# Kernel optimization log

Hardware: AMD Instinct MI355X
Metric: run time of the kernel (lower is better)

Reference implementation:

```python
import jax, jax.numpy as jnp
import numpy as np

B = 16384      # batch
H = 1024       # latent_dim
C = 2          # output_dim (classes)
PPC = 24       # prototypes per class
P = C * PPC    # 48 total prototypes
EPS = 1e-4


def setup_inputs() -> dict:
    key = jax.random.key(0)
    k1, k2, k3, k4, k5 = jax.random.split(key, 5)
    specific_user = jax.random.normal(k1, (B, H), jnp.float32)
    shared_user = jax.random.normal(k2, (B, H), jnp.float32)
    prototype_vectors = jax.random.normal(k3, (P, H), jnp.float32)
    # last_layer weight set by set_last_layer_incorrect_connection(-0.5):
    # +1 for the prototype's own class, -0.5 elsewhere; shape [C, P]
    cls = np.arange(P) // PPC
    ident = (cls[None, :] == np.arange(C)[:, None]).astype(np.float32)
    last_layer_w = jnp.asarray(ident * 1.0 + (1.0 - ident) * (-0.5))
    # nn.Bilinear(H, H, 1): weight [1, H, H], bias [1]
    bilinear_w = jax.random.normal(k4, (1, H, H), jnp.float32) / np.sqrt(H)
    bilinear_b = jax.random.normal(k5, (1,), jnp.float32) * 0.01
    return {
        "specific_user": specific_user,
        "shared_user": shared_user,
        "prototype_vectors": prototype_vectors,
        "last_layer_w": last_layer_w,
        "bilinear_w": bilinear_w,
        "bilinear_b": bilinear_b,
        "flag": 1,
    }


def reference(specific_user, shared_user, prototype_vectors, last_layer_w,
              bilinear_w, bilinear_b, flag):
    # prototype_distances: squared euclid via mm + norms, then log-similarity
    x2 = jnp.sum(specific_user ** 2, axis=1, keepdims=True)          # [B,1]
    p2 = jnp.sum(prototype_vectors ** 2, axis=1)                     # [P]
    distance = -2.0 * (specific_user @ prototype_vectors.T) + x2 + p2[None, :]  # [B,P]
    similarity = jnp.log((distance + 1.0) / (distance + EPS))        # [B,P]
    logits = similarity @ last_layer_w.T                             # [B,C]

    # select the class's 24 prototypes (flag picks class 1 or 0; static int)
    idx = 1 if flag else 0
    sub = prototype_vectors.reshape(C, PPC, H)[idx]                  # [PPC,H]

    # prototype_subgraph_distances: per original broadcast, each row of
    # all_sim is the batch-mean of the log-similarity -> constant over batch.
    s2 = jnp.sum(sub ** 2, axis=1)                                   # [PPC]
    d = -2.0 * (specific_user @ sub.T) + x2 + s2[None, :]            # [B,PPC]
    sim = jnp.mean(jnp.log((d + 1.0) / (d + EPS)), axis=0)           # [PPC]
    jstar = jnp.argmax(sim)                                          # scalar
    chosen_proto = jnp.broadcast_to(sub[jstar], specific_user.shape) # [B,H]

    # nn.Bilinear(chosen_proto, shared_user) -> [B,1]
    pos = jnp.einsum('bi,ij,bj->b', chosen_proto, bilinear_w[0], shared_user)[:, None] + bilinear_b
    return (pos, shared_user, logits, distance)
```

## Files before the change

kernel.cpp:

```cpp
#include <hip/hip_runtime.h>
#include <hip/hip_bf16.h>

#define BATCH 16384
#define HD    1024
#define NP    48
#define PPC   24
#define EPSV  1e-4f

typedef __attribute__((ext_vector_type(8))) short  short8;
typedef __attribute__((ext_vector_type(4))) float  floatx4;

__device__ __forceinline__ float b2f(unsigned short s) {
    union { unsigned u; float f; } c; c.u = ((unsigned)s) << 16; return c.f;
}
__device__ __forceinline__ unsigned short f2bu(float f) {
    __hip_bfloat16 h = __float2bfloat16(f);
    union { __hip_bfloat16 h; unsigned short u; } c; c.h = h; return c.u;
}

__global__ __launch_bounds__(64) void k_prep(const float* __restrict__ proto,
                                             unsigned short* __restrict__ phi,
                                             unsigned short* __restrict__ plo,
                                             float* __restrict__ p2) {
    const int p = blockIdx.x;
    const int lane = threadIdx.x;
    const float* row = proto + (size_t)p * HD;
    float acc = 0.f;
    for (int k = lane; k < HD; k += 64) {
        const float f = row[k];
        acc += f * f;
        const unsigned short h = f2bu(f);
        phi[(size_t)p * HD + k] = h;
        plo[(size_t)p * HD + k] = f2bu(f - b2f(h));
    }
#pragma unroll
    for (int m = 32; m >= 1; m >>= 1) acc += __shfl_xor(acc, m, 64);
    if (lane == 0) p2[p] = acc;
}

__global__ __launch_bounds__(256) void k_main(
    const float* __restrict__ x,
    const unsigned short* __restrict__ phi,
    const unsigned short* __restrict__ plo,
    const float* __restrict__ llw,
    const float* __restrict__ p2,
    float* __restrict__ partials,
    float* __restrict__ out_logits,
    float* __restrict__ out_dist)
{
    __shared__ float cs[NP];
    const int wave = threadIdx.x >> 6;
    const int lane = threadIdx.x & 63;
    const int quad = lane >> 4;
    const int lr   = lane & 15;
    const int rb   = (blockIdx.x * 4 + wave) * 16;

    if (threadIdx.x < NP) cs[threadIdx.x] = 0.f;
    __syncthreads();

    const float* xr = x + (size_t)(rb + lr) * HD + quad * 8;
    const unsigned short* ph0 = phi + (size_t)lr * HD + quad * 8;
    const unsigned short* ph1 = ph0 + 16 * HD;
    const unsigned short* ph2 = ph0 + 32 * HD;
    const unsigned short* pl0 = plo + (size_t)lr * HD + quad * 8;
    const unsigned short* pl1 = pl0 + 16 * HD;
    const unsigned short* pl2 = pl0 + 32 * HD;

    floatx4 acc0 = {0.f, 0.f, 0.f, 0.f};
    floatx4 acc1 = {0.f, 0.f, 0.f, 0.f};
    floatx4 acc2 = {0.f, 0.f, 0.f, 0.f};
    float x2p = 0.f;

#pragma unroll 2
    for (int kk = 0; kk < 32; ++kk) {
        const floatx4 xa = *(const floatx4*)(xr + kk * 32);
        const floatx4 xb = *(const floatx4*)(xr + kk * 32 + 4);
        short8 ah, al;
#pragma unroll
        for (int j = 0; j < 4; ++j) {
            const float f = xa[j];
            x2p += f * f;
            const unsigned short h = f2bu(f);
            ah[j] = (short)h;
            al[j] = (short)f2bu(f - b2f(h));
        }
#pragma unroll
        for (int j = 0; j < 4; ++j) {
            const float f = xb[j];
            x2p += f * f;
            const unsigned short h = f2bu(f);
            ah[4 + j] = (short)h;
            al[4 + j] = (short)f2bu(f - b2f(h));
        }
        const short8 bh0 = *(const short8*)(ph0 + kk * 32);
        const short8 bh1 = *(const short8*)(ph1 + kk * 32);
        const short8 bh2 = *(const short8*)(ph2 + kk * 32);
        const short8 bl0 = *(const short8*)(pl0 + kk * 32);
        const short8 bl1 = *(const short8*)(pl1 + kk * 32);
        const short8 bl2 = *(const short8*)(pl2 + kk * 32);
        acc0 = __builtin_amdgcn_mfma_f32_16x16x32_bf16(ah, bh0, acc0, 0, 0, 0);
        acc0 = __builtin_amdgcn_mfma_f32_16x16x32_bf16(ah, bl0, acc0, 0, 0, 0);
        acc0 = __builtin_amdgcn_mfma_f32_16x16x32_bf16(al, bh0, acc0, 0, 0, 0);
        acc1 = __builtin_amdgcn_mfma_f32_16x16x32_bf16(ah, bh1, acc1, 0, 0, 0);
        acc1 = __builtin_amdgcn_mfma_f32_16x16x32_bf16(ah, bl1, acc1, 0, 0, 0);
        acc1 = __builtin_amdgcn_mfma_f32_16x16x32_bf16(al, bh1, acc1, 0, 0, 0);
        acc2 = __builtin_amdgcn_mfma_f32_16x16x32_bf16(ah, bh2, acc2, 0, 0, 0);
        acc2 = __builtin_amdgcn_mfma_f32_16x16x32_bf16(ah, bl2, acc2, 0, 0, 0);
        acc2 = __builtin_amdgcn_mfma_f32_16x16x32_bf16(al, bh2, acc2, 0, 0, 0);
    }
    x2p += __shfl_xor(x2p, 16, 64);
    x2p += __shfl_xor(x2p, 32, 64);

    float s0[4] = {0.f, 0.f, 0.f, 0.f};
    float s1[4] = {0.f, 0.f, 0.f, 0.f};
    floatx4 accs[3] = {acc0, acc1, acc2};

#pragma unroll
    for (int t = 0; t < 3; ++t) {
        const int p = t * 16 + lr;
        const float p2p = p2[p];
        const float w0 = llw[p];
        const float w1 = llw[NP + p];
        float cst = 0.f;
#pragma unroll
        for (int r = 0; r < 4; ++r) {
            const int row = quad * 4 + r;
            const float x2r = __shfl(x2p, row, 64);
            const float d = -2.f * accs[t][r] + x2r + p2p;
            out_dist[(size_t)(rb + row) * NP + p] = d;
            const float sim = log1pf((1.f - EPSV) / (d + EPSV));
            s0[r] += sim * w0;
            s1[r] += sim * w1;
            cst += sim;
        }
        cst += __shfl_xor(cst, 16, 64);
        cst += __shfl_xor(cst, 32, 64);
        if (quad == 0) atomicAdd(&cs[p], cst);
    }

#pragma unroll
    for (int r = 0; r < 4; ++r) {
        float r0 = s0[r], r1 = s1[r];
#pragma unroll
        for (int m = 1; m <= 8; m <<= 1) {
            r0 += __shfl_xor(r0, m, 64);
            r1 += __shfl_xor(r1, m, 64);
        }
        if (lr == 0) {
            const int brow = rb + quad * 4 + r;
            out_logits[(size_t)brow * 2 + 0] = r0;
            out_logits[(size_t)brow * 2 + 1] = r1;
        }
    }

    __syncthreads();
    if (threadIdx.x < NP) partials[(size_t)blockIdx.x * NP + threadIdx.x] = cs[threadIdx.x];
}

__global__ __launch_bounds__(256) void k_matvec(
    const float* __restrict__ proto,
    const float* __restrict__ w2,
    const float* __restrict__ partials,
    const int* __restrict__ flag,
    float* __restrict__ v)
{
    __shared__ float colsum[PPC];
    __shared__ int js;
    const int tid = threadIdx.x;
    const int idx = (flag[0] != 0) ? 1 : 0;
    if (tid < PPC) {
        float s = 0.f;
        for (int blk = 0; blk < 256; ++blk)
            s += partials[(size_t)blk * NP + idx * PPC + tid];
        colsum[tid] = s;
    }
    __syncthreads();
    if (tid == 0) {
        int bj = 0; float bv = colsum[0];
        for (int j = 1; j < PPC; ++j)
            if (colsum[j] > bv) { bv = colsum[j]; bj = j; }
        js = bj;
    }
    __syncthreads();

    const float* crow = proto + (size_t)(idx * PPC + js) * HD;
    const int i0 = blockIdx.x * 64;
    const int j4 = tid * 4;
    float a0 = 0.f, a1 = 0.f, a2 = 0.f, a3 = 0.f;
    for (int i = i0; i < i0 + 64; ++i) {
        const float c = crow[i];
        const floatx4 wv = *(const floatx4*)(w2 + (size_t)i * HD + j4);
        a0 += c * wv[0];
        a1 += c * wv[1];
        a2 += c * wv[2];
        a3 += c * wv[3];
    }
    atomicAdd(&v[j4 + 0], a0);
    atomicAdd(&v[j4 + 1], a1);
    atomicAdd(&v[j4 + 2], a2);
    atomicAdd(&v[j4 + 3], a3);
}

__global__ __launch_bounds__(256) void k_pos(
    const float* __restrict__ sh,
    const float* __restrict__ v,
    const float* __restrict__ bias,
    float* __restrict__ out_pos,
    float* __restrict__ out_copy)
{
    const int wave = threadIdx.x >> 6;
    const int lane = threadIdx.x & 63;
    const int b = blockIdx.x * 4 + wave;

    const floatx4* src = (const floatx4*)(sh + (size_t)b * HD);
    floatx4* dst = (floatx4*)(out_copy + (size_t)b * HD);
    const float* vp = v + lane * 16;
    float acc = 0.f;
#pragma unroll
    for (int c = 0; c < 4; ++c) {
        const floatx4 r = src[lane * 4 + c];
        dst[lane * 4 + c] = r;
#pragma unroll
        for (int j = 0; j < 4; ++j) acc += r[j] * vp[c * 4 + j];
    }
#pragma unroll
    for (int m = 1; m <= 32; m <<= 1) acc += __shfl_xor(acc, m, 64);
    if (lane == 0) out_pos[b] = acc + bias[0];
}

extern "C" void kernel_launch(void* const* d_in, const int* in_sizes, int n_in,
                              void* d_out, int out_size, void* d_ws, size_t ws_size,
                              hipStream_t stream) {
    const float* x     = (const float*)d_in[0];
    const float* sh    = (const float*)d_in[1];
    const float* proto = (const float*)d_in[2];
    const float* llw   = (const float*)d_in[3];
    const float* w2    = (const float*)d_in[4];
    const float* bb    = (const float*)d_in[5];
    const int*   flag  = (const int*)d_in[6];

    float* out = (float*)d_out;
    float* out_pos    = out;
    float* out_copy   = out + BATCH;
    float* out_logits = out + BATCH + BATCH * HD;
    float* out_dist   = out + BATCH + BATCH * HD + BATCH * 2;

    float* ws_v    = (float*)d_ws;
    float* ws_p2   = ws_v + 1024;
    float* ws_part = ws_v + 1088;
    unsigned short* ws_phi = (unsigned short*)(ws_v + 16384);
    unsigned short* ws_plo = ws_phi + NP * HD;

    hipMemsetAsync(d_ws, 0, 1024 * sizeof(float), stream);
    k_prep<<<48, 64, 0, stream>>>(proto, ws_phi, ws_plo, ws_p2);
    k_main<<<256, 256, 0, stream>>>(x, ws_phi, ws_plo, llw, ws_p2, ws_part, out_logits, out_dist);
    k_matvec<<<16, 256, 0, stream>>>(proto, w2, ws_part, flag, ws_v);
    k_pos<<<4096, 256, 0, stream>>>(sh, ws_v, bb, out_pos, out_copy);
}
```

Baseline: 231.6 us.

## Split k_main over K across waves with LDS reduction and global column atomics

k_main now gives each block 16 rows and splits the 1024-wide reduction across its four waves. The partial MFMA accumulators and squared norms are reduced through LDS, and wave 0 finishes the epilogue. The grid grows from 256 to 1024 blocks to raise parallelism and memory-level concurrency. Per-block column partials become direct global atomics, so k_matvec no longer scans partials. k_matvec uses 64 blocks instead of 16, and k_pos switches to coalesced lane-contiguous indexing with nontemporal stores for the large copy. The costs are more float atomics, which make the column sums nondeterministic, and three idle waves during the epilogue.

```diff
diff --git a/kernel.cpp b/kernel.cpp
--- a/kernel.cpp
+++ b/kernel.cpp
@@ -38,31 +38,30 @@
     if (lane == 0) p2[p] = acc;
 }
 
-__global__ __launch_bounds__(256) void k_main(
+__global__ __launch_bounds__(256, 4) void k_main(
     const float* __restrict__ x,
     const unsigned short* __restrict__ phi,
     const unsigned short* __restrict__ plo,
     const float* __restrict__ llw,
     const float* __restrict__ p2,
-    float* __restrict__ partials,
+    float* __restrict__ gcol,
     float* __restrict__ out_logits,
     float* __restrict__ out_dist)
 {
-    __shared__ float cs[NP];
+    __shared__ float lacc[4][64][13];
+    __shared__ float lx2[4][16];
     const int wave = threadIdx.x >> 6;
     const int lane = threadIdx.x & 63;
     const int quad = lane >> 4;
     const int lr   = lane & 15;
-    const int rb   = (blockIdx.x * 4 + wave) * 16;
-
-    if (threadIdx.x < NP) cs[threadIdx.x] = 0.f;
-    __syncthreads();
-
-    const float* xr = x + (size_t)(rb + lr) * HD + quad * 8;
-    const unsigned short* ph0 = phi + (size_t)lr * HD + quad * 8;
+    const int rb   = blockIdx.x * 16;
+    const int ko   = wave * 256;
+
+    const float* xr = x + (size_t)(rb + lr) * HD + ko + quad * 8;
+    const unsigned short* ph0 = phi + (size_t)lr * HD + ko + quad * 8;
     const unsigned short* ph1 = ph0 + 16 * HD;
     const unsigned short* ph2 = ph0 + 32 * HD;
-    const unsigned short* pl0 = plo + (size_t)lr * HD + quad * 8;
+    const unsigned short* pl0 = plo + (size_t)lr * HD + ko + quad * 8;
     const unsigned short* pl1 = pl0 + 16 * HD;
     const unsigned short* pl2 = pl0 + 32 * HD;
 
@@ -72,7 +71,7 @@
     float x2p = 0.f;
 
 #pragma unroll 2
-    for (int kk = 0; kk < 32; ++kk) {
+    for (int kk = 0; kk < 8; ++kk) {
         const floatx4 xa = *(const floatx4*)(xr + kk * 32);
         const floatx4 xb = *(const floatx4*)(xr + kk * 32 + 4);
         short8 ah, al;
@@ -111,9 +110,24 @@
     x2p += __shfl_xor(x2p, 16, 64);
     x2p += __shfl_xor(x2p, 32, 64);
 
+#pragma unroll
+    for (int r = 0; r < 4; ++r) {
+        lacc[wave][lane][r]     = acc0[r];
+        lacc[wave][lane][4 + r] = acc1[r];
+        lacc[wave][lane][8 + r] = acc2[r];
+    }
+    if (quad == 0) lx2[wave][lr] = x2p;
+    __syncthreads();
+    if (wave != 0) return;
+
+    float facc[12];
+#pragma unroll
+    for (int i = 0; i < 12; ++i)
+        facc[i] = lacc[0][lane][i] + lacc[1][lane][i] + lacc[2][lane][i] + lacc[3][lane][i];
+    const float x2full = lx2[0][lr] + lx2[1][lr] + lx2[2][lr] + lx2[3][lr];
+
     float s0[4] = {0.f, 0.f, 0.f, 0.f};
     float s1[4] = {0.f, 0.f, 0.f, 0.f};
-    floatx4 accs[3] = {acc0, acc1, acc2};
 
 #pragma unroll
     for (int t = 0; t < 3; ++t) {
@@ -125,8 +139,8 @@
 #pragma unroll
         for (int r = 0; r < 4; ++r) {
             const int row = quad * 4 + r;
-            const float x2r = __shfl(x2p, row, 64);
-            const float d = -2.f * accs[t][r] + x2r + p2p;
+            const float x2r = __shfl(x2full, row, 64);
+            const float d = -2.f * facc[t * 4 + r] + x2r + p2p;
             out_dist[(size_t)(rb + row) * NP + p] = d;
             const float sim = log1pf((1.f - EPSV) / (d + EPSV));
             s0[r] += sim * w0;
@@ -135,7 +149,7 @@
         }
         cst += __shfl_xor(cst, 16, 64);
         cst += __shfl_xor(cst, 32, 64);
-        if (quad == 0) atomicAdd(&cs[p], cst);
+        if (quad == 0) atomicAdd(&gcol[p], cst);
     }
 
 #pragma unroll
@@ -152,42 +166,33 @@
             out_logits[(size_t)brow * 2 + 1] = r1;
         }
     }
-
-    __syncthreads();
-    if (threadIdx.x < NP) partials[(size_t)blockIdx.x * NP + threadIdx.x] = cs[threadIdx.x];
 }
 
 __global__ __launch_bounds__(256) void k_matvec(
     const float* __restrict__ proto,
     const float* __restrict__ w2,
-    const float* __restrict__ partials,
+    const float* __restrict__ gcol,
     const int* __restrict__ flag,
     float* __restrict__ v)
 {
-    __shared__ float colsum[PPC];
     __shared__ int js;
     const int tid = threadIdx.x;
     const int idx = (flag[0] != 0) ? 1 : 0;
-    if (tid < PPC) {
-        float s = 0.f;
-        for (int blk = 0; blk < 256; ++blk)
-            s += partials[(size_t)blk * NP + idx * PPC + tid];
-        colsum[tid] = s;
+    if (tid == 0) {
+        const float* cs = gcol + idx * PPC;
+        int bj = 0; float bv = cs[0];
+        for (int j = 1; j < PPC; ++j)
+            if (cs[j] > bv) { bv = cs[j]; bj = j; }
+        js = bj;
     }
     __syncthreads();
-    if (tid == 0) {
-        int bj = 0; float bv = colsum[0];
-        for (int j = 1; j < PPC; ++j)
-            if (colsum[j] > bv) { bv = colsum[j]; bj = j; }
-        js = bj;
-    }
-    __syncthreads();
 
     const float* crow = proto + (size_t)(idx * PPC + js) * HD;
-    const int i0 = blockIdx.x * 64;
+    const int i0 = blockIdx.x * 16;
     const int j4 = tid * 4;
     float a0 = 0.f, a1 = 0.f, a2 = 0.f, a3 = 0.f;
-    for (int i = i0; i < i0 + 64; ++i) {
+#pragma unroll 4
+    for (int i = i0; i < i0 + 16; ++i) {
         const float c = crow[i];
         const floatx4 wv = *(const floatx4*)(w2 + (size_t)i * HD + j4);
         a0 += c * wv[0];
@@ -214,14 +219,16 @@
 
     const floatx4* src = (const floatx4*)(sh + (size_t)b * HD);
     floatx4* dst = (floatx4*)(out_copy + (size_t)b * HD);
-    const float* vp = v + lane * 16;
+    const floatx4* vv = (const floatx4*)v;
     float acc = 0.f;
 #pragma unroll
     for (int c = 0; c < 4; ++c) {
-        const floatx4 r = src[lane * 4 + c];
-        dst[lane * 4 + c] = r;
-#pragma unroll
-        for (int j = 0; j < 4; ++j) acc += r[j] * vp[c * 4 + j];
+        const int idx = c * 64 + lane;
+        const floatx4 r = src[idx];
+        __builtin_nontemporal_store(r, &dst[idx]);
+        const floatx4 vr = vv[idx];
+#pragma unroll
+        for (int j = 0; j < 4; ++j) acc += r[j] * vr[j];
     }
 #pragma unroll
     for (int m = 1; m <= 32; m <<= 1) acc += __shfl_xor(acc, m, 64);
@@ -246,14 +253,14 @@
     float* out_dist   = out + BATCH + BATCH * HD + BATCH * 2;
 
     float* ws_v    = (float*)d_ws;
-    float* ws_p2   = ws_v + 1024;
-    float* ws_part = ws_v + 1088;
+    float* ws_col  = ws_v + 1024;
+    float* ws_p2   = ws_v + 1088;
     unsigned short* ws_phi = (unsigned short*)(ws_v + 16384);
     unsigned short* ws_plo = ws_phi + NP * HD;
 
-    hipMemsetAsync(d_ws, 0, 1024 * sizeof(float), stream);
+    hipMemsetAsync(d_ws, 0, 8192, stream);
     k_prep<<<48, 64, 0, stream>>>(proto, ws_phi, ws_plo, ws_p2);
-    k_main<<<256, 256, 0, stream>>>(x, ws_phi, ws_plo, llw, ws_p2, ws_part, out_logits, out_dist);
-    k_matvec<<<16, 256, 0, stream>>>(proto, w2, ws_part, flag, ws_v);
+    k_main<<<1024, 256, 0, stream>>>(x, ws_phi, ws_plo, llw, ws_p2, ws_col, out_logits, out_dist);
+    k_matvec<<<64, 256, 0, stream>>>(proto, w2, ws_col, flag, ws_v);
     k_pos<<<4096, 256, 0, stream>>>(sh, ws_v, bb, out_pos, out_copy);
 }
```

Measured after the change: 228.8 us. Within noise of the previous version (-1.2%).
